# Optimization experiments

Hardware: AMD Instinct MI355X
Metric: run time of the kernel (lower is better)

Reference implementation:

```python
import jax, jax.numpy as jnp
import numpy as np

PRE_HEIGHT = 96
PRE_WIDTH = 128


def setup_inputs() -> dict:
    key = jax.random.key(0)
    B, K, H, W = 32, 64, 96, 128
    x = jax.random.normal(key, (B, K, H, W), dtype=jnp.float32)
    return {"combined_hm_preds": x, "batch_size": B, "num_of_kp": K}


def reference(combined_hm_preds, batch_size, num_of_kp):
    B, K, H, W = combined_hm_preds.shape
    # nn.Softmax() with no dim on a 4D tensor -> softmax over dim=1 (channels)
    map_val_all = jax.nn.softmax(combined_hm_preds, axis=1)
    # zeta[b,k] = sum over spatial of the channel-softmaxed map
    get_zeta = map_val_all.sum(axis=(2, 3))  # [B, K]
    js = jnp.arange(W, dtype=map_val_all.dtype)
    iis = jnp.arange(H, dtype=map_val_all.dtype)
    # per-channel weighted coordinate sums
    Sx = jnp.einsum('bkij,j->bk', map_val_all, js)  # [B, K]
    Sy = jnp.einsum('bkij,i->bk', map_val_all, iis)  # [B, K]
    # faithful to the original: accumulators are never reset across k or b,
    # so each keypoint uses the inclusive cumulative sum in flattened (b,k) order
    cum_x = jnp.cumsum(Sx.reshape(-1)).reshape(B, K)
    cum_y = jnp.cumsum(Sy.reshape(-1)).reshape(B, K)
    kx = jnp.round(cum_x / get_zeta)
    ky = jnp.round(cum_y / get_zeta)
    # out-of-range clamp to the image center, as in the original
    kx = jnp.where((kx > PRE_WIDTH) | (kx < 0), PRE_WIDTH * 0.5, kx)
    ky = jnp.where((ky > PRE_HEIGHT) | (ky < 0), PRE_HEIGHT * 0.5, ky)
    keypoint = jnp.stack([kx, ky], axis=-1)  # [B, K, 2]
    return (map_val_all, keypoint, get_zeta)
```

## Files before the change

kernel.cpp:

```cpp
#include <hip/hip_runtime.h>
#include <math.h>

#define BB 32
#define KK 64
#define HH 96
#define WW 128
#define HW (HH*WW)
#define MAP_SIZE (BB*KK*HW)
#define NBK (BB*KK)
#define NT  (HW/256)

__global__ __launch_bounds__(256) void fused_k(const float* __restrict__ x,
                                               float* __restrict__ out,
                                               double* __restrict__ sxyz) {
    __shared__ float  sm[KK][257];
    __shared__ float  dinv[256];
    __shared__ double pz[4][64], px[4][64], py[4][64];

    int blk  = blockIdx.x;
    int b    = blk / NT;
    int tile = blk - b * NT;
    int t    = threadIdx.x;
    size_t base = (size_t)b * KK * HW + (size_t)tile * 256 + t;

    float den = 0.f;
    #pragma unroll
    for (int k = 0; k < KK; ++k) {
        float e = __expf(x[base + (size_t)k * HW]);
        sm[k][t] = e;
        den += e;
    }
    float inv = 1.f / den;
    dinv[t] = inv;

    #pragma unroll
    for (int k = 0; k < KK; ++k) {
        out[base + (size_t)k * HW] = sm[k][t] * inv;
    }

    __syncthreads();

    int k = t & 63, chunk = t >> 6;
    int p0 = chunk * 64;
    double z = 0.0, sx = 0.0, sy = 0.0;
    #pragma unroll
    for (int j = 0; j < 64; ++j) {
        int p = p0 + j;
        double m = (double)(sm[k][p] * dinv[p]);
        int g = tile * 256 + p;
        z  += m;
        sx += m * (double)(g & (WW - 1));
        sy += m * (double)(g >> 7);
    }
    pz[chunk][k] = z; px[chunk][k] = sx; py[chunk][k] = sy;
    __syncthreads();

    if (t < 64) {
        double Z  = pz[0][t] + pz[1][t] + pz[2][t] + pz[3][t];
        double SX = px[0][t] + px[1][t] + px[2][t] + px[3][t];
        double SY = py[0][t] + py[1][t] + py[2][t] + py[3][t];
        int bk = b * KK + t;
        atomicAdd(&sxyz[bk * 3 + 0], SX);
        atomicAdd(&sxyz[bk * 3 + 1], SY);
        atomicAdd(&sxyz[bk * 3 + 2], Z);
    }
}

__global__ __launch_bounds__(256) void keypoint_k(const double* __restrict__ sxyz,
                                                  float* __restrict__ kp,
                                                  float* __restrict__ zeta) {
    const int PT = NBK / 256;
    int t = threadIdx.x;
    int lane = t & 63, wid = t >> 6;

    double vx[PT], vy[PT];
    double cx = 0.0, cy = 0.0;
    #pragma unroll
    for (int e = 0; e < PT; ++e) {
        int idx = t * PT + e;
        cx += sxyz[idx * 3 + 0]; vx[e] = cx;
        cy += sxyz[idx * 3 + 1]; vy[e] = cy;
    }
    double tx = cx, ty = cy;
    for (int off = 1; off < 64; off <<= 1) {
        double ax = __shfl_up(tx, off, 64);
        double ay = __shfl_up(ty, off, 64);
        if (lane >= off) { tx += ax; ty += ay; }
    }
    __shared__ double wxs[4], wys[4];
    if (lane == 63) { wxs[wid] = tx; wys[wid] = ty; }
    __syncthreads();
    double offx = tx - cx, offy = ty - cy;
    for (int w2 = 0; w2 < wid; ++w2) { offx += wxs[w2]; offy += wys[w2]; }

    #pragma unroll
    for (int e = 0; e < PT; ++e) {
        int idx = t * PT + e;
        double zz = sxyz[idx * 3 + 2];
        double kx = rint((vx[e] + offx) / zz);
        double ky = rint((vy[e] + offy) / zz);
        float fkx = (float)kx, fky = (float)ky;
        if (fkx > 128.0f || fkx < 0.0f) fkx = 64.0f;
        if (fky > 96.0f  || fky < 0.0f) fky = 48.0f;
        kp[idx * 2 + 0] = fkx;
        kp[idx * 2 + 1] = fky;
        zeta[idx] = (float)zz;
    }
}

extern "C" void kernel_launch(void* const* d_in, const int* in_sizes, int n_in,
                              void* d_out, int out_size, void* d_ws, size_t ws_size,
                              hipStream_t stream) {
    const float* x = (const float*)d_in[0];
    float* out  = (float*)d_out;
    float* map  = out;
    float* kp   = out + MAP_SIZE;
    float* zeta = out + MAP_SIZE + NBK * 2;
    double* sxyz = (double*)d_ws;

    hipMemsetAsync(d_ws, 0, (size_t)NBK * 3 * sizeof(double), stream);
    fused_k   <<< BB * NT, 256, 0, stream >>> (x, map, sxyz);
    keypoint_k<<< 1,       256, 0, stream >>> (sxyz, kp, zeta);
}
```

Baseline: 188.8 us.

## Keep exp values in registers and reduce from re-read output via shuffles

Removes the large shared-memory staging buffer by keeping per-pixel exponentials in registers, freeing LDS so more blocks can reside per CU. The coordinate/zeta reduction now re-reads the freshly written softmax map from global memory with float4 loads and reduces across 4 lanes with shuffles, dropping the second barrier and shared partials. Input loads become nontemporal. This trades LDS pressure for extra global (likely L2-resident) read traffic and higher register use.

```diff
diff --git a/kernel.cpp b/kernel.cpp
--- a/kernel.cpp
+++ b/kernel.cpp
@@ -10,59 +10,56 @@
 #define NBK (BB*KK)
 #define NT  (HW/256)
 
-__global__ __launch_bounds__(256) void fused_k(const float* __restrict__ x,
-                                               float* __restrict__ out,
-                                               double* __restrict__ sxyz) {
-    __shared__ float  sm[KK][257];
-    __shared__ float  dinv[256];
-    __shared__ double pz[4][64], px[4][64], py[4][64];
-
+__global__ __launch_bounds__(256, 4) void fused_k(const float* __restrict__ x,
+                                                  float* __restrict__ out,
+                                                  double* __restrict__ sxyz) {
     int blk  = blockIdx.x;
     int b    = blk / NT;
     int tile = blk - b * NT;
     int t    = threadIdx.x;
-    size_t base = (size_t)b * KK * HW + (size_t)tile * 256 + t;
+    size_t base = (size_t)b * (KK * HW) + (size_t)tile * 256 + t;
 
+    float e[KK];
     float den = 0.f;
     #pragma unroll
     for (int k = 0; k < KK; ++k) {
-        float e = __expf(x[base + (size_t)k * HW]);
-        sm[k][t] = e;
-        den += e;
+        e[k] = __expf(__builtin_nontemporal_load(&x[base + (size_t)k * HW]));
+        den += e[k];
     }
     float inv = 1.f / den;
-    dinv[t] = inv;
 
     #pragma unroll
     for (int k = 0; k < KK; ++k) {
-        out[base + (size_t)k * HW] = sm[k][t] * inv;
+        out[base + (size_t)k * HW] = e[k] * inv;
     }
 
     __syncthreads();
 
-    int k = t & 63, chunk = t >> 6;
-    int p0 = chunk * 64;
+    int k = t >> 2;
+    int q = t & 3;
+    const float* mp = out + (size_t)b * (KK * HW) + (size_t)k * HW + tile * 256;
+    const double gy_base = (double)(tile * 2);
     double z = 0.0, sx = 0.0, sy = 0.0;
     #pragma unroll
-    for (int j = 0; j < 64; ++j) {
-        int p = p0 + j;
-        double m = (double)(sm[k][p] * dinv[p]);
-        int g = tile * 256 + p;
-        z  += m;
-        sx += m * (double)(g & (WW - 1));
-        sy += m * (double)(g >> 7);
+    for (int j = 0; j < 16; ++j) {
+        int p = q * 4 + j * 16;
+        float4 v = *reinterpret_cast<const float4*>(mp + p);
+        double m0 = (double)v.x, m1 = (double)v.y, m2 = (double)v.z, m3 = (double)v.w;
+        double s = ((m0 + m1) + m2) + m3;
+        double gx0 = (double)(p & (WW - 1));
+        z  += s;
+        sx += s * gx0 + (m1 + 2.0 * m2 + 3.0 * m3);
+        sy += s * (gy_base + (double)(p >> 7));
     }
-    pz[chunk][k] = z; px[chunk][k] = sx; py[chunk][k] = sy;
-    __syncthreads();
 
-    if (t < 64) {
-        double Z  = pz[0][t] + pz[1][t] + pz[2][t] + pz[3][t];
-        double SX = px[0][t] + px[1][t] + px[2][t] + px[3][t];
-        double SY = py[0][t] + py[1][t] + py[2][t] + py[3][t];
-        int bk = b * KK + t;
-        atomicAdd(&sxyz[bk * 3 + 0], SX);
-        atomicAdd(&sxyz[bk * 3 + 1], SY);
-        atomicAdd(&sxyz[bk * 3 + 2], Z);
+    z  += __shfl_xor(z,  1, 64);  z  += __shfl_xor(z,  2, 64);
+    sx += __shfl_xor(sx, 1, 64);  sx += __shfl_xor(sx, 2, 64);
+    sy += __shfl_xor(sy, 1, 64);  sy += __shfl_xor(sy, 2, 64);
+    if (q == 0) {
+        int bk = b * KK + k;
+        atomicAdd(&sxyz[bk * 3 + 0], sx);
+        atomicAdd(&sxyz[bk * 3 + 1], sy);
+        atomicAdd(&sxyz[bk * 3 + 2], z);
     }
 }
 
@@ -73,13 +70,14 @@
     int t = threadIdx.x;
     int lane = t & 63, wid = t >> 6;
 
-    double vx[PT], vy[PT];
+    double vx[PT], vy[PT], vz[PT];
     double cx = 0.0, cy = 0.0;
     #pragma unroll
     for (int e = 0; e < PT; ++e) {
         int idx = t * PT + e;
         cx += sxyz[idx * 3 + 0]; vx[e] = cx;
         cy += sxyz[idx * 3 + 1]; vy[e] = cy;
+        vz[e] = sxyz[idx * 3 + 2];
     }
     double tx = cx, ty = cy;
     for (int off = 1; off < 64; off <<= 1) {
@@ -96,7 +94,7 @@
     #pragma unroll
     for (int e = 0; e < PT; ++e) {
         int idx = t * PT + e;
-        double zz = sxyz[idx * 3 + 2];
+        double zz = vz[e];
         double kx = rint((vx[e] + offx) / zz);
         double ky = rint((vy[e] + offy) / zz);
         float fkx = (float)kx, fky = (float)ky;
```

After: 188.1 us. No clear change (-0.4%).

## Vectorize softmax with float2 nontemporal I/O and restructure per-channel reductions

Applied to the files above, without the earlier changes.

Each thread now handles two pixels through float2 nontemporal loads and stores, so a 128-thread block covers the same 256-pixel tile. The spatial reduction is split into 8-channel chunks staged through small shared buffers, reduced with wave shuffles, and the x/y weights are derived algebraically from pixel-pair sums. This aims to raise memory efficiency on the bandwidth-bound map write and cut shared-memory traffic and double-precision work. The cost is more __syncthreads per block and smaller blocks, which may hurt occupancy.

```diff
diff --git a/kernel.cpp b/kernel.cpp
--- a/kernel.cpp
+++ b/kernel.cpp
@@ -8,61 +8,80 @@
 #define HW (HH*WW)
 #define MAP_SIZE (BB*KK*HW)
 #define NBK (BB*KK)
-#define NT  (HW/256)
+#define TPX 256
+#define NT3 (HW/TPX)
+#define NTHR 128
 
-__global__ __launch_bounds__(256) void fused_k(const float* __restrict__ x,
-                                               float* __restrict__ out,
-                                               double* __restrict__ sxyz) {
-    __shared__ float  sm[KK][257];
-    __shared__ float  dinv[256];
-    __shared__ double pz[4][64], px[4][64], py[4][64];
+typedef float f32x2 __attribute__((ext_vector_type(2)));
+
+__global__ __launch_bounds__(NTHR) void fused_k(const float* __restrict__ x,
+                                                float* __restrict__ out,
+                                                double* __restrict__ sxyz) {
+    __shared__ f32x2 smv[KK][NTHR];
+    __shared__ float zc[8][NTHR + 1];
+    __shared__ float wc[8][NTHR + 1];
 
     int blk  = blockIdx.x;
-    int b    = blk / NT;
-    int tile = blk - b * NT;
+    int b    = blk / NT3;
+    int tile = blk - b * NT3;
     int t    = threadIdx.x;
-    size_t base = (size_t)b * KK * HW + (size_t)tile * 256 + t;
+    size_t base2 = ((size_t)b * (KK * HW) + (size_t)tile * TPX) / 2 + t;
+    const f32x2* xp = reinterpret_cast<const f32x2*>(x);
+    f32x2*       op = reinterpret_cast<f32x2*>(out);
 
-    float den = 0.f;
+    float d0 = 0.f, d1 = 0.f;
     #pragma unroll
     for (int k = 0; k < KK; ++k) {
-        float e = __expf(x[base + (size_t)k * HW]);
-        sm[k][t] = e;
-        den += e;
+        f32x2 v = __builtin_nontemporal_load(xp + base2 + (size_t)k * (HW / 2));
+        f32x2 e;
+        e.x = __expf(v.x);
+        e.y = __expf(v.y);
+        smv[k][t] = e;
+        d0 += e.x; d1 += e.y;
     }
-    float inv = 1.f / den;
-    dinv[t] = inv;
+    float i0 = 1.f / d0, i1 = 1.f / d1;
+
+    int ci = t & 7, g = t >> 3;
+    const double gxb = (double)((g * 16) & (WW - 1));
+    const double gy  = (double)(tile * (TPX / WW) + (g >> 3));
 
     #pragma unroll
-    for (int k = 0; k < KK; ++k) {
-        out[base + (size_t)k * HW] = sm[k][t] * inv;
-    }
+    for (int c = 0; c < 8; ++c) {
+        #pragma unroll
+        for (int ki = 0; ki < 8; ++ki) {
+            int k = c * 8 + ki;
+            f32x2 e = smv[k][t];
+            f32x2 m;
+            m.x = e.x * i0;
+            m.y = e.y * i1;
+            __builtin_nontemporal_store(m, op + base2 + (size_t)k * (HW / 2));
+            zc[ki][t] = m.x + m.y;
+            wc[ki][t] = m.y;
+        }
+        __syncthreads();
 
-    __syncthreads();
+        double Z = 0.0, W = 0.0;
+        #pragma unroll
+        for (int j = 0; j < 8; ++j) {
+            int s = g * 8 + j;
+            double z = (double)zc[ci][s];
+            double w = (double)wc[ci][s];
+            Z += z;
+            W += (double)(2 * j) * z + w;
+        }
+        double SX = gxb * Z + W;
+        double SY = gy * Z;
 
-    int k = t & 63, chunk = t >> 6;
-    int p0 = chunk * 64;
-    double z = 0.0, sx = 0.0, sy = 0.0;
-    #pragma unroll
-    for (int j = 0; j < 64; ++j) {
-        int p = p0 + j;
-        double m = (double)(sm[k][p] * dinv[p]);
-        int g = tile * 256 + p;
-        z  += m;
-        sx += m * (double)(g & (WW - 1));
-        sy += m * (double)(g >> 7);
-    }
-    pz[chunk][k] = z; px[chunk][k] = sx; py[chunk][k] = sy;
-    __syncthreads();
-
-    if (t < 64) {
-        double Z  = pz[0][t] + pz[1][t] + pz[2][t] + pz[3][t];
-        double SX = px[0][t] + px[1][t] + px[2][t] + px[3][t];
-        double SY = py[0][t] + py[1][t] + py[2][t] + py[3][t];
-        int bk = b * KK + t;
-        atomicAdd(&sxyz[bk * 3 + 0], SX);
-        atomicAdd(&sxyz[bk * 3 + 1], SY);
-        atomicAdd(&sxyz[bk * 3 + 2], Z);
+        Z  += __shfl_xor(Z,  8, 64); Z  += __shfl_xor(Z,  16, 64); Z  += __shfl_xor(Z,  32, 64);
+        SX += __shfl_xor(SX, 8, 64); SX += __shfl_xor(SX, 16, 64); SX += __shfl_xor(SX, 32, 64);
+        SY += __shfl_xor(SY, 8, 64); SY += __shfl_xor(SY, 16, 64); SY += __shfl_xor(SY, 32, 64);
+        if ((t & 63) < 8) {
+            int bk = b * KK + c * 8 + ci;
+            atomicAdd(&sxyz[bk * 3 + 0], SX);
+            atomicAdd(&sxyz[bk * 3 + 1], SY);
+            atomicAdd(&sxyz[bk * 3 + 2], Z);
+        }
+        __syncthreads();
     }
 }
 
@@ -73,13 +92,14 @@
     int t = threadIdx.x;
     int lane = t & 63, wid = t >> 6;
 
-    double vx[PT], vy[PT];
+    double vx[PT], vy[PT], vz[PT];
     double cx = 0.0, cy = 0.0;
     #pragma unroll
     for (int e = 0; e < PT; ++e) {
         int idx = t * PT + e;
         cx += sxyz[idx * 3 + 0]; vx[e] = cx;
         cy += sxyz[idx * 3 + 1]; vy[e] = cy;
+        vz[e] = sxyz[idx * 3 + 2];
     }
     double tx = cx, ty = cy;
     for (int off = 1; off < 64; off <<= 1) {
@@ -96,7 +116,7 @@
     #pragma unroll
     for (int e = 0; e < PT; ++e) {
         int idx = t * PT + e;
-        double zz = sxyz[idx * 3 + 2];
+        double zz = vz[e];
         double kx = rint((vx[e] + offx) / zz);
         double ky = rint((vy[e] + offy) / zz);
         float fkx = (float)kx, fky = (float)ky;
@@ -119,6 +139,6 @@
     double* sxyz = (double*)d_ws;
 
     hipMemsetAsync(d_ws, 0, (size_t)NBK * 3 * sizeof(double), stream);
-    fused_k   <<< BB * NT, 256, 0, stream >>> (x, map, sxyz);
-    keypoint_k<<< 1,       256, 0, stream >>> (sxyz, kp, zeta);
+    fused_k   <<< BB * NT3, NTHR, 0, stream >>> (x, map, sxyz);
+    keypoint_k<<< 1,        256,  0, stream >>> (sxyz, kp, zeta);
 }
```

Result: slower. 196.7 us (+4.2%).
